# Kernel tuning notes

Measured on AMD Instinct MI355X. Metric: run time of the kernel, lower is better.

Reference implementation:

```python
import jax, jax.numpy as jnp
import numpy as np

IN_DIM = 1024
OUT_DIM = 1024
NUM_COEFFS = 32 + 3  # grid_size + spline_order


def setup_inputs() -> dict:
    key = jax.random.key(0)
    k1, k2, k3 = jax.random.split(key, 3)
    x = jax.random.normal(k1, (4096, IN_DIM), dtype=jnp.float32)
    spline_weight = jax.random.normal(k2, (IN_DIM, OUT_DIM, NUM_COEFFS), dtype=jnp.float32) * 0.1
    base_scale = jax.random.normal(k3, (IN_DIM, OUT_DIM), dtype=jnp.float32) * 0.1
    grid = jnp.linspace(-1.0, 1.0, NUM_COEFFS, dtype=jnp.float32)
    return {"x": x, "spline_weight": spline_weight, "base_scale": base_scale, "grid": grid}


def _b_spline_cubic(x, grid):
    # x: [b, i] -> basis [b, i, c]
    h = 2.0 / (NUM_COEFFS - 1)
    dist = jnp.abs(x[..., None] - grid) / h
    inner = 2.0 / 3.0 - dist * dist + dist * dist * dist * 0.5
    t = 2.0 - dist
    outer = t * t * t / 6.0
    return jnp.where(dist < 1.0, inner, jnp.where(dist < 2.0, outer, 0.0))


def reference(x, spline_weight, base_scale, grid):
    x_norm = jnp.clip(x, -0.99, 0.99)
    base_act = jax.nn.silu(x_norm)                      # [b, i]
    base_out = jnp.einsum('bi,ij->bj', base_act, base_scale)
    basis = _b_spline_cubic(x_norm, grid)               # [b, i, c]
    spline_out = jnp.einsum('bic,ijc->bj', basis, spline_weight)
    return base_out + spline_out
```

## Files before the change

### kernel.cpp

```cpp
#include <hip/hip_runtime.h>
#include <hip/hip_bf16.h>


#define IN_DIM 1024
#define OUT_DIM 1024
#define NC 35
#define KPI 36
#define KTOT (IN_DIM * KPI)
#define NW (KTOT / 32)
#define MROWS 4096
#define BM 256
#define BN 256
#define BK 32
#define NSPLIT 4
#define WPC (NW / NSPLIT)

typedef __attribute__((ext_vector_type(8))) __bf16 bf16x8;
typedef __attribute__((ext_vector_type(4))) float f32x4;

__device__ __forceinline__ unsigned short f2bf(float f) {
  unsigned int u = __builtin_bit_cast(unsigned int, f);
  u = (u + 0x7FFFu + ((u >> 16) & 1u)) >> 16;
  return (unsigned short)u;
}

__global__ __launch_bounds__(256) void prep_w(const float* __restrict__ sw,
                                              const float* __restrict__ bs,
                                              unsigned short* __restrict__ w2) {
  __shared__ float sbuf[2][256 * NC];
  const int tid = threadIdx.x;
  const int w = blockIdx.x;
  const int n0 = blockIdx.y * 256;
  const int k0 = w * 32;
  const int i0 = k0 / KPI;
  const int i1 = (k0 + 31) / KPI;
  const int iq[2] = {i0, i1};
  float bsv[2];
#pragma unroll
  for (int q = 0; q < 2; ++q) {
    const float* src = sw + ((size_t)iq[q] * OUT_DIM + n0) * NC;
    for (int t = tid; t < 256 * NC; t += 256) sbuf[q][t] = src[t];
    bsv[q] = bs[(size_t)iq[q] * OUT_DIM + n0 + tid];
  }
  __syncthreads();
  unsigned short v[32];
#pragma unroll
  for (int kk = 0; kk < 32; ++kk) {
    int k = k0 + kk;
    int q = (k >= (i0 + 1) * KPI) ? 1 : 0;
    int c = k - iq[q] * KPI;
    float f = (c < NC) ? sbuf[q][tid * NC + c] : bsv[q];
    v[kk] = f2bf(f);
  }
  uint4* dst = (uint4*)(w2 + ((size_t)w * OUT_DIM + n0 + tid) * 32);
#pragma unroll
  for (int j = 0; j < 4; ++j) {
    uint4 t4;
    t4.x = (unsigned)v[8 * j + 0] | ((unsigned)v[8 * j + 1] << 16);
    t4.y = (unsigned)v[8 * j + 2] | ((unsigned)v[8 * j + 3] << 16);
    t4.z = (unsigned)v[8 * j + 4] | ((unsigned)v[8 * j + 5] << 16);
    t4.w = (unsigned)v[8 * j + 6] | ((unsigned)v[8 * j + 7] << 16);
    dst[j] = t4;
  }
}

__global__ __launch_bounds__(256) void prep_a2(const float* __restrict__ x,
                                               unsigned short* __restrict__ a2) {
  const int tid = threadIdx.x;
  const int w = blockIdx.x;
  const int b = blockIdx.y * 256 + tid;
  const int k0 = w * 32;
  const int i0 = k0 / KPI;
  const int i1 = (k0 + 31) / KPI;
  const int iq[2] = {i0, i1};
  int si[2];
  float tv0[2], tv1[2], tv2[2], tv3[2], sg[2];
#pragma unroll
  for (int q = 0; q < 2; ++q) {
    float xv = x[(size_t)b * IN_DIM + iq[q]];
    float xn = fminf(fmaxf(xv, -0.99f), 0.99f);
    float u = (xn + 1.0f) * 17.0f;
    float sf = floorf(u);
    si[q] = (int)sf;
    float f = u - sf, g = 1.0f - f;
    float f2 = f * f, g2 = g * g;
    tv0[q] = g2 * g * (1.f / 6.f);
    tv1[q] = 0.66666667f - f2 + 0.5f * f2 * f;
    tv2[q] = 0.66666667f - g2 + 0.5f * g2 * g;
    tv3[q] = f2 * f * (1.f / 6.f);
    sg[q] = xn / (1.0f + __expf(-xn));
  }
  unsigned short v[32];
#pragma unroll
  for (int kk = 0; kk < 32; ++kk) {
    int k = k0 + kk;
    int q = (k >= (i0 + 1) * KPI) ? 1 : 0;
    int c = k - iq[q] * KPI;
    float val;
    if (c == NC) {
      val = sg[q];
    } else {
      int rel = c - (si[q] - 1);
      val = (rel == 0) ? tv0[q]
          : (rel == 1) ? tv1[q]
          : (rel == 2) ? tv2[q]
          : (rel == 3) ? tv3[q] : 0.0f;
    }
    v[kk] = f2bf(val);
  }
  uint4* dst = (uint4*)(a2 + ((size_t)w * MROWS + b) * 32);
#pragma unroll
  for (int j = 0; j < 4; ++j) {
    uint4 t4;
    t4.x = (unsigned)v[8 * j + 0] | ((unsigned)v[8 * j + 1] << 16);
    t4.y = (unsigned)v[8 * j + 2] | ((unsigned)v[8 * j + 3] << 16);
    t4.z = (unsigned)v[8 * j + 4] | ((unsigned)v[8 * j + 5] << 16);
    t4.w = (unsigned)v[8 * j + 6] | ((unsigned)v[8 * j + 7] << 16);
    dst[j] = t4;
  }
}

__global__ __launch_bounds__(512) void kan_gemm3(const unsigned short* __restrict__ A2,
                                                 const unsigned short* __restrict__ W2,
                                                 float* __restrict__ out) {
  __shared__ __align__(16) unsigned short As[3][BM * BK];
  __shared__ __align__(16) unsigned short Ws[3][BN * BK];

  const int tid = threadIdx.x;
  const int mt = blockIdx.x, nt = blockIdx.y, kc = blockIdx.z;

  const int lane = tid & 63;
  const int wid = tid >> 6;
  const int wm = (wid & 3) * 64;
  const int wn = (wid >> 2) * 128;
  const int lm = lane & 15;
  const int quad = lane >> 4;
  const int ko = quad * 8;

  f32x4 acc[4][8];
#pragma unroll
  for (int a = 0; a < 4; ++a)
#pragma unroll
    for (int b = 0; b < 8; ++b) acc[a][b] = f32x4{0.f, 0.f, 0.f, 0.f};

  const unsigned short* Abase = A2 + (size_t)(mt * BM) * 32 + lane * 8;
  const unsigned short* Wbase = W2 + (size_t)(nt * BN) * 32 + lane * 8;

  auto issue = [&](int buf, int w) {
    const size_t aoff = (size_t)w * (MROWS * 32);
    const size_t woff = (size_t)w * (OUT_DIM * 32);
#pragma unroll
    for (int c = 0; c < 2; ++c) {
      const int g = wid * 2 + c;
      __builtin_amdgcn_global_load_lds(
          (const __attribute__((address_space(1))) unsigned int*)(Abase + aoff + (size_t)g * 512),
          (__attribute__((address_space(3))) unsigned int*)(&As[buf][g * 512]),
          16, 0, 0);
      __builtin_amdgcn_global_load_lds(
          (const __attribute__((address_space(1))) unsigned int*)(Wbase + woff + (size_t)g * 512),
          (__attribute__((address_space(3))) unsigned int*)(&Ws[buf][g * 512]),
          16, 0, 0);
    }
  };

  issue(0, kc * WPC);
  int cur = 0, nxt = 1;
  for (int step = 0; step < WPC; ++step) {
    if (step + 1 < WPC) {
      issue(nxt, kc * WPC + step + 1);
      asm volatile("s_waitcnt vmcnt(4) lgkmcnt(0)\ns_barrier" ::: "memory");
    } else {
      asm volatile("s_waitcnt vmcnt(0) lgkmcnt(0)\ns_barrier" ::: "memory");
    }

    uint4 af[4];
#pragma unroll
    for (int mi = 0; mi < 4; ++mi)
      af[mi] = *(const uint4*)(&As[cur][(wm + mi * 16 + lm) * BK + ko]);
#pragma unroll
    for (int h = 0; h < 2; ++h) {
      uint4 bfr[4];
#pragma unroll
      for (int nj = 0; nj < 4; ++nj)
        bfr[nj] = *(const uint4*)(&Ws[cur][(wn + h * 64 + nj * 16 + lm) * BK + ko]);
#pragma unroll
      for (int mi = 0; mi < 4; ++mi)
#pragma unroll
        for (int nj = 0; nj < 4; ++nj)
          acc[mi][h * 4 + nj] = __builtin_amdgcn_mfma_f32_16x16x32_bf16(
              __builtin_bit_cast(bf16x8, af[mi]), __builtin_bit_cast(bf16x8, bfr[nj]),
              acc[mi][h * 4 + nj], 0, 0, 0);
    }

    cur = nxt;
    nxt = (nxt == 2) ? 0 : nxt + 1;
  }

#pragma unroll
  for (int mi = 0; mi < 4; ++mi)
#pragma unroll
    for (int ni = 0; ni < 8; ++ni)
#pragma unroll
      for (int r = 0; r < 4; ++r) {
        int row = mt * BM + wm + mi * 16 + quad * 4 + r;
        int col = nt * BN + wn + ni * 16 + lm;
        atomicAdd(&out[(size_t)row * OUT_DIM + col], acc[mi][ni][r]);
      }
}

#define FB_BM 128
#define FB_BN 128
#define FB_BKPA 40
#define FB_KCH 9216
#define FB_NSTEP 288

__global__ __launch_bounds__(256) void prep_wb_fb(const float* __restrict__ sw,
                                                  const float* __restrict__ bs,
                                                  unsigned short* __restrict__ wb) {
  int id = blockIdx.x * 256 + threadIdx.x;
  int i = id & (IN_DIM - 1);
  int n = id >> 10;
  const float* s = sw + (size_t)i * (OUT_DIM * NC) + (size_t)n * NC;
  unsigned short v[KPI];
#pragma unroll
  for (int c = 0; c < NC; ++c) v[c] = f2bf(s[c]);
  v[NC] = f2bf(bs[(size_t)i * OUT_DIM + n]);
  uint2* dst = (uint2*)(wb + (size_t)n * KTOT + (size_t)i * KPI);
#pragma unroll
  for (int w = 0; w < 9; ++w) {
    uint2 t;
    t.x = (unsigned)v[4 * w + 0] | ((unsigned)v[4 * w + 1] << 16);
    t.y = (unsigned)v[4 * w + 2] | ((unsigned)v[4 * w + 3] << 16);
    dst[w] = t;
  }
}

template <bool USE_WB>
__global__ __launch_bounds__(256) void kan_gemm_fb(const float* __restrict__ x,
                                                   const unsigned short* __restrict__ wb,
                                                   const float* __restrict__ sw,
                                                   const float* __restrict__ bs,
                                                   float* __restrict__ out) {
  __shared__ __align__(16) unsigned short As[FB_BM * FB_BKPA];
  __shared__ __align__(16) unsigned short Wsm[FB_BN * FB_BKPA];

  const int tid = threadIdx.x;
  const int mt = blockIdx.x, nt = blockIdx.y, kc = blockIdx.z;
  const int sb = tid & 127;
  const int shalf = tid >> 7;
  const int klo = shalf * 16;
  const int wrow = tid >> 1;
  const int whal = tid & 1;
  const int lane = tid & 63;
  const int wid = tid >> 6;
  const int wm = (wid & 1) * 64;
  const int wn = (wid >> 1) * 64;
  const int lm = lane & 15;
  const int quad = lane >> 4;
  const int ko = quad * 8;

  f32x4 acc[4][4];
#pragma unroll
  for (int a = 0; a < 4; ++a)
#pragma unroll
    for (int b = 0; b < 4; ++b) acc[a][b] = f32x4{0.f, 0.f, 0.f, 0.f};

  const float* xrow = x + (size_t)(mt * FB_BM + sb) * IN_DIM;

  for (int step = 0; step < FB_NSTEP; ++step) {
    const int kbase = kc * FB_KCH + step * BK;
    {
      uint4 z = make_uint4(0, 0, 0, 0);
      uint4* az = (uint4*)(&As[sb * FB_BKPA + klo]);
      az[0] = z;
      az[1] = z;
    }
    {
      const int ilo = kbase / KPI;
      const int ihi = (kbase + BK - 1) / KPI;
      for (int ii = ilo; ii <= ihi; ++ii) {
        float xv = xrow[ii];
        float xn = fminf(fmaxf(xv, -0.99f), 0.99f);
        float u = (xn + 1.0f) * 17.0f;
        float sf = floorf(u);
        int s = (int)sf;
        float f = u - sf, g = 1.0f - f;
        float f2 = f * f, g2 = g * g;
        float v0 = g2 * g * (1.f / 6.f);
        float v1 = 0.66666667f - f2 + 0.5f * f2 * f;
        float v2 = 0.66666667f - g2 + 0.5f * g2 * g;
        float v3 = f2 * f * (1.f / 6.f);
        float sig = xn / (1.0f + __expf(-xn));
        const int kb0 = ii * KPI - kbase;
#pragma unroll
        for (int t = 0; t < 4; ++t) {
          int c = s - 1 + t;
          float v = (t == 0) ? v0 : (t == 1) ? v1 : (t == 2) ? v2 : v3;
          int kq = kb0 + c;
          if (c >= 0 && c < NC && kq >= klo && kq < klo + 16)
            As[sb * FB_BKPA + kq] = f2bf(v);
        }
        int kqb = kb0 + NC;
        if (kqb >= klo && kqb < klo + 16) As[sb * FB_BKPA + kqb] = f2bf(sig);
      }
    }
    if (USE_WB) {
      const unsigned short* src = wb + (size_t)(nt * FB_BN + wrow) * KTOT + kbase + whal * 16;
      uint4 w0 = ((const uint4*)src)[0];
      uint4 w1 = ((const uint4*)src)[1];
      uint4* wd = (uint4*)(&Wsm[wrow * FB_BKPA + whal * 16]);
      wd[0] = w0;
      wd[1] = w1;
    } else {
      const int j = nt * FB_BN + wrow;
      unsigned int p[8];
#pragma unroll
      for (int q = 0; q < 8; ++q) {
        unsigned int lohi = 0;
#pragma unroll
        for (int h = 0; h < 2; ++h) {
          int k = kbase + whal * 16 + q * 2 + h;
          int i = k / KPI;
          int c = k - i * KPI;
          float v = (c < NC) ? sw[(size_t)i * (OUT_DIM * NC) + (size_t)j * NC + c]
                             : bs[(size_t)i * OUT_DIM + j];
          lohi |= ((unsigned int)f2bf(v)) << (16 * h);
        }
        p[q] = lohi;
      }
      uint4* wd = (uint4*)(&Wsm[wrow * FB_BKPA + whal * 16]);
      wd[0] = make_uint4(p[0], p[1], p[2], p[3]);
      wd[1] = make_uint4(p[4], p[5], p[6], p[7]);
    }

    __syncthreads();

    uint4 af[4], bfr[4];
#pragma unroll
    for (int mi = 0; mi < 4; ++mi)
      af[mi] = *(const uint4*)(&As[(wm + mi * 16 + lm) * FB_BKPA + ko]);
#pragma unroll
    for (int ni = 0; ni < 4; ++ni)
      bfr[ni] = *(const uint4*)(&Wsm[(wn + ni * 16 + lm) * FB_BKPA + ko]);
#pragma unroll
    for (int mi = 0; mi < 4; ++mi)
#pragma unroll
      for (int ni = 0; ni < 4; ++ni)
        acc[mi][ni] = __builtin_amdgcn_mfma_f32_16x16x32_bf16(
            __builtin_bit_cast(bf16x8, af[mi]), __builtin_bit_cast(bf16x8, bfr[ni]),
            acc[mi][ni], 0, 0, 0);

    __syncthreads();
  }

#pragma unroll
  for (int mi = 0; mi < 4; ++mi)
#pragma unroll
    for (int ni = 0; ni < 4; ++ni)
#pragma unroll
      for (int r = 0; r < 4; ++r) {
        int row = mt * FB_BM + wm + mi * 16 + quad * 4 + r;
        int col = nt * FB_BN + wn + ni * 16 + lm;
        atomicAdd(&out[(size_t)row * OUT_DIM + col], acc[mi][ni][r]);
      }
}

extern "C" void kernel_launch(void* const* d_in, const int* in_sizes, int n_in,
                              void* d_out, int out_size, void* d_ws, size_t ws_size,
                              hipStream_t stream) {
  const float* x = (const float*)d_in[0];
  const float* sw = (const float*)d_in[1];
  const float* bs = (const float*)d_in[2];
  float* out = (float*)d_out;

  hipMemsetAsync(d_out, 0, (size_t)MROWS * OUT_DIM * sizeof(float), stream);

  const size_t WB_BYTES = (size_t)NW * OUT_DIM * 32 * sizeof(unsigned short);
  const size_t A_BYTES = (size_t)NW * MROWS * 32 * sizeof(unsigned short);

  if (ws_size >= WB_BYTES + A_BYTES) {
    unsigned short* w2 = (unsigned short*)d_ws;
    unsigned short* a2 = (unsigned short*)((char*)d_ws + WB_BYTES);
    prep_w<<<dim3(NW, OUT_DIM / 256), 256, 0, stream>>>(sw, bs, w2);
    prep_a2<<<dim3(NW, MROWS / 256), 256, 0, stream>>>(x, a2);
    kan_gemm3<<<dim3(MROWS / BM, OUT_DIM / BN, NSPLIT), 512, 0, stream>>>(a2, w2, out);
  } else if (ws_size >= WB_BYTES) {
    unsigned short* wbp = (unsigned short*)d_ws;
    prep_wb_fb<<<(IN_DIM * OUT_DIM) / 256, 256, 0, stream>>>(sw, bs, wbp);
    kan_gemm_fb<true><<<dim3(32, 8, 4), 256, 0, stream>>>(x, wbp, sw, bs, out);
  } else {
    kan_gemm_fb<false><<<dim3(32, 8, 4), 256, 0, stream>>>(x, nullptr, sw, bs, out);
  }
}
```

Before: 719.6 us.

## Swizzle bf16 operand layout, restructure prep kernels to cut LDS conflicts

Operand packing now XOR-swizzles each row's four 16-byte chunks by row index, and the GEMM reads LDS fragments with the matching swizzled offset to reduce LDS bank conflicts. The weight prep kernel drops the shared-memory staging and reads spline weights directly from global memory. The activation prep kernel now handles 8 inputs (9 K-chunks) per thread, loading x with float4 and computing basis values once instead of per 32-wide chunk. The direct strided weight reads may coalesce less well than the staged version.

```diff
diff --git a/kernel.cpp b/kernel.cpp
--- a/kernel.cpp
+++ b/kernel.cpp
@@ -24,103 +24,104 @@
   return (unsigned short)u;
 }
 
-__global__ __launch_bounds__(256) void prep_w(const float* __restrict__ sw,
-                                              const float* __restrict__ bs,
-                                              unsigned short* __restrict__ w2) {
-  __shared__ float sbuf[2][256 * NC];
+__device__ __forceinline__ uint4 pack8(const unsigned short* v) {
+  uint4 t4;
+  t4.x = (unsigned)v[0] | ((unsigned)v[1] << 16);
+  t4.y = (unsigned)v[2] | ((unsigned)v[3] << 16);
+  t4.z = (unsigned)v[4] | ((unsigned)v[5] << 16);
+  t4.w = (unsigned)v[6] | ((unsigned)v[7] << 16);
+  return t4;
+}
+
+__global__ __launch_bounds__(256) void prep_w2(const float* __restrict__ sw,
+                                               const float* __restrict__ bs,
+                                               unsigned short* __restrict__ w2) {
   const int tid = threadIdx.x;
   const int w = blockIdx.x;
-  const int n0 = blockIdx.y * 256;
+  const int n = blockIdx.y * 256 + tid;
   const int k0 = w * 32;
   const int i0 = k0 / KPI;
-  const int i1 = (k0 + 31) / KPI;
-  const int iq[2] = {i0, i1};
-  float bsv[2];
-#pragma unroll
-  for (int q = 0; q < 2; ++q) {
-    const float* src = sw + ((size_t)iq[q] * OUT_DIM + n0) * NC;
-    for (int t = tid; t < 256 * NC; t += 256) sbuf[q][t] = src[t];
-    bsv[q] = bs[(size_t)iq[q] * OUT_DIM + n0 + tid];
-  }
-  __syncthreads();
+  const int off0 = k0 - i0 * KPI;
+  const int split = (KPI - off0 < 32) ? (KPI - off0) : 32;
+  const int i1 = (i0 + 1 < IN_DIM) ? (i0 + 1) : i0;
+  const float* p0 = sw + ((size_t)i0 * OUT_DIM + n) * NC;
+  const float* p1 = sw + ((size_t)i1 * OUT_DIM + n) * NC;
+  const float bsv = bs[(size_t)i0 * OUT_DIM + n];
+  const int swz = (tid >> 1) & 3;
+
   unsigned short v[32];
 #pragma unroll
   for (int kk = 0; kk < 32; ++kk) {
-    int k = k0 + kk;
-    int q = (k >= (i0 + 1) * KPI) ? 1 : 0;
-    int c = k - iq[q] * KPI;
-    float f = (c < NC) ? sbuf[q][tid * NC + c] : bsv[q];
-    v[kk] = f2bf(f);
-  }
-  uint4* dst = (uint4*)(w2 + ((size_t)w * OUT_DIM + n0 + tid) * 32);
-#pragma unroll
-  for (int j = 0; j < 4; ++j) {
-    uint4 t4;
-    t4.x = (unsigned)v[8 * j + 0] | ((unsigned)v[8 * j + 1] << 16);
-    t4.y = (unsigned)v[8 * j + 2] | ((unsigned)v[8 * j + 3] << 16);
-    t4.z = (unsigned)v[8 * j + 4] | ((unsigned)v[8 * j + 5] << 16);
-    t4.w = (unsigned)v[8 * j + 6] | ((unsigned)v[8 * j + 7] << 16);
-    dst[j] = t4;
-  }
-}
-
-__global__ __launch_bounds__(256) void prep_a2(const float* __restrict__ x,
-                                               unsigned short* __restrict__ a2) {
+    const int c = off0 + kk;
+    const bool ph0 = (kk < split);
+    const float* base = ph0 ? p0 : p1;
+    const int idx = ph0 ? (c < NC ? c : 0) : (kk - split);
+    float fv = base[idx];
+    if (ph0 && c == NC) fv = bsv;
+    v[kk] = f2bf(fv);
+  }
+  uint4* dst = (uint4*)(w2 + ((size_t)w * OUT_DIM + n) * 32);
+#pragma unroll
+  for (int j = 0; j < 4; ++j) dst[j ^ swz] = pack8(&v[8 * j]);
+}
+
+__global__ __launch_bounds__(256) void prep_a2t(const float* __restrict__ x,
+                                                unsigned short* __restrict__ a2) {
   const int tid = threadIdx.x;
-  const int w = blockIdx.x;
+  const int g = blockIdx.x;
   const int b = blockIdx.y * 256 + tid;
-  const int k0 = w * 32;
-  const int i0 = k0 / KPI;
-  const int i1 = (k0 + 31) / KPI;
-  const int iq[2] = {i0, i1};
-  int si[2];
-  float tv0[2], tv1[2], tv2[2], tv3[2], sg[2];
-#pragma unroll
-  for (int q = 0; q < 2; ++q) {
-    float xv = x[(size_t)b * IN_DIM + iq[q]];
-    float xn = fminf(fmaxf(xv, -0.99f), 0.99f);
+  const int i0 = g * 8;
+  const int w0 = g * 9;
+  const int swz = (tid >> 1) & 3;
+
+  float4 xa = *(const float4*)(x + (size_t)b * IN_DIM + i0);
+  float4 xb = *(const float4*)(x + (size_t)b * IN_DIM + i0 + 4);
+  const float xv[8] = {xa.x, xa.y, xa.z, xa.w, xb.x, xb.y, xb.z, xb.w};
+
+  int si[8];
+  unsigned short tb0[8], tb1[8], tb2[8], tb3[8], sgb[8];
+#pragma unroll
+  for (int q = 0; q < 8; ++q) {
+    float xn = fminf(fmaxf(xv[q], -0.99f), 0.99f);
     float u = (xn + 1.0f) * 17.0f;
     float sf = floorf(u);
     si[q] = (int)sf;
-    float f = u - sf, g = 1.0f - f;
-    float f2 = f * f, g2 = g * g;
-    tv0[q] = g2 * g * (1.f / 6.f);
-    tv1[q] = 0.66666667f - f2 + 0.5f * f2 * f;
-    tv2[q] = 0.66666667f - g2 + 0.5f * g2 * g;
-    tv3[q] = f2 * f * (1.f / 6.f);
-    sg[q] = xn / (1.0f + __expf(-xn));
-  }
-  unsigned short v[32];
-#pragma unroll
-  for (int kk = 0; kk < 32; ++kk) {
-    int k = k0 + kk;
-    int q = (k >= (i0 + 1) * KPI) ? 1 : 0;
-    int c = k - iq[q] * KPI;
-    float val;
-    if (c == NC) {
-      val = sg[q];
-    } else {
-      int rel = c - (si[q] - 1);
-      val = (rel == 0) ? tv0[q]
-          : (rel == 1) ? tv1[q]
-          : (rel == 2) ? tv2[q]
-          : (rel == 3) ? tv3[q] : 0.0f;
-    }
-    v[kk] = f2bf(val);
-  }
-  uint4* dst = (uint4*)(a2 + ((size_t)w * MROWS + b) * 32);
-#pragma unroll
-  for (int j = 0; j < 4; ++j) {
-    uint4 t4;
-    t4.x = (unsigned)v[8 * j + 0] | ((unsigned)v[8 * j + 1] << 16);
-    t4.y = (unsigned)v[8 * j + 2] | ((unsigned)v[8 * j + 3] << 16);
-    t4.z = (unsigned)v[8 * j + 4] | ((unsigned)v[8 * j + 5] << 16);
-    t4.w = (unsigned)v[8 * j + 6] | ((unsigned)v[8 * j + 7] << 16);
-    dst[j] = t4;
-  }
-}
-
-__global__ __launch_bounds__(512) void kan_gemm3(const unsigned short* __restrict__ A2,
+    float f = u - sf, gg = 1.0f - f;
+    float f2 = f * f, g2 = gg * gg;
+    tb0[q] = f2bf(g2 * gg * (1.f / 6.f));
+    tb1[q] = f2bf(0.66666667f - f2 + 0.5f * f2 * f);
+    tb2[q] = f2bf(0.66666667f - g2 + 0.5f * g2 * gg);
+    tb3[q] = f2bf(f2 * f * (1.f / 6.f));
+    sgb[q] = f2bf(xn / (1.0f + __expf(-xn)));
+  }
+
+#pragma unroll
+  for (int wl = 0; wl < 9; ++wl) {
+    unsigned short v[32];
+#pragma unroll
+    for (int kk = 0; kk < 32; ++kk) {
+      const int kr = wl * 32 + kk;
+      const int q = kr / KPI;
+      const int c = kr % KPI;
+      unsigned short val;
+      if (c == NC) {
+        val = sgb[q];
+      } else {
+        int rel = c - (si[q] - 1);
+        val = (rel == 0) ? tb0[q]
+            : (rel == 1) ? tb1[q]
+            : (rel == 2) ? tb2[q]
+            : (rel == 3) ? tb3[q] : (unsigned short)0;
+      }
+      v[kk] = val;
+    }
+    uint4* dst = (uint4*)(a2 + ((size_t)(w0 + wl) * MROWS + b) * 32);
+#pragma unroll
+    for (int j = 0; j < 4; ++j) dst[j ^ swz] = pack8(&v[8 * j]);
+  }
+}
+
+__global__ __launch_bounds__(512) void kan_gemm5(const unsigned short* __restrict__ A2,
                                                  const unsigned short* __restrict__ W2,
                                                  float* __restrict__ out) {
   __shared__ __align__(16) unsigned short As[3][BM * BK];
@@ -135,7 +136,7 @@
   const int wn = (wid >> 2) * 128;
   const int lm = lane & 15;
   const int quad = lane >> 4;
-  const int ko = quad * 8;
+  const int koS = (quad ^ ((lm >> 1) & 3)) * 8;
 
   f32x4 acc[4][8];
 #pragma unroll
@@ -176,13 +177,13 @@
     uint4 af[4];
 #pragma unroll
     for (int mi = 0; mi < 4; ++mi)
-      af[mi] = *(const uint4*)(&As[cur][(wm + mi * 16 + lm) * BK + ko]);
+      af[mi] = *(const uint4*)(&As[cur][(wm + mi * 16 + lm) * BK + koS]);
 #pragma unroll
     for (int h = 0; h < 2; ++h) {
       uint4 bfr[4];
 #pragma unroll
       for (int nj = 0; nj < 4; ++nj)
-        bfr[nj] = *(const uint4*)(&Ws[cur][(wn + h * 64 + nj * 16 + lm) * BK + ko]);
+        bfr[nj] = *(const uint4*)(&Ws[cur][(wn + h * 64 + nj * 16 + lm) * BK + koS]);
 #pragma unroll
       for (int mi = 0; mi < 4; ++mi)
 #pragma unroll
@@ -381,9 +382,9 @@
   if (ws_size >= WB_BYTES + A_BYTES) {
     unsigned short* w2 = (unsigned short*)d_ws;
     unsigned short* a2 = (unsigned short*)((char*)d_ws + WB_BYTES);
-    prep_w<<<dim3(NW, OUT_DIM / 256), 256, 0, stream>>>(sw, bs, w2);
-    prep_a2<<<dim3(NW, MROWS / 256), 256, 0, stream>>>(x, a2);
-    kan_gemm3<<<dim3(MROWS / BM, OUT_DIM / BN, NSPLIT), 512, 0, stream>>>(a2, w2, out);
+    prep_w2<<<dim3(NW, OUT_DIM / 256), 256, 0, stream>>>(sw, bs, w2);
+    prep_a2t<<<dim3(KTOT / 288, MROWS / 256), 256, 0, stream>>>(x, a2);
+    kan_gemm5<<<dim3(MROWS / BM, OUT_DIM / BN, NSPLIT), 512, 0, stream>>>(a2, w2, out);
   } else if (ws_size >= WB_BYTES) {
     unsigned short* wbp = (unsigned short*)d_ws;
     prep_wb_fb<<<(IN_DIM * OUT_DIM) / 256, 256, 0, stream>>>(sw, bs, wbp);
```

Measured after the change: 707.8 us. No clear change (-1.6%).
